# Optimization experiments

Hardware: AMD Instinct MI355X
Metric: run time of the kernel (lower is better)

The kernel has to match this reference:

```python
import jax, jax.numpy as jnp
import numpy as np

H = 1024
S = 8192
B = 1  # module's broadcast in the weighted-sum step only supports B == 1


def setup_inputs() -> dict:
    key = jax.random.key(0)
    k1, k2, k3 = jax.random.split(key, 3)
    scale = 1.0 / np.sqrt(H)
    enc_out = jax.random.normal(k1, (B, S, H), dtype=jnp.float32)
    w1 = jax.random.normal(k2, (H, H), dtype=jnp.float32) * scale  # nn.Linear weight [out,in]
    w2 = jax.random.normal(k3, (H, H), dtype=jnp.float32) * scale
    return {"enc_out": enc_out, "w1": w1, "w2": w2}


def reference(enc_out, w1, w2):
    # attn_weights = tanh(w1(enc_out)) @ w2(enc_out)^T  -> [B, S, S]
    q = jnp.tanh(jnp.einsum('bsh,oh->bso', enc_out, w1))
    k = jnp.einsum('bsh,oh->bso', enc_out, w2)
    scores = jnp.einsum('bih,bjh->bij', q, k)          # [B, S, S]
    attn = jax.nn.softmax(scores, axis=1)               # softmax over dim=1 (rows)
    # torch: sum over dim=1 of attn[B,S,S,1] * enc_out broadcast as [1,B,S,H].
    # For B==1 this equals enc_out[0,j,h] * sum_i attn[0,i,j]; avoid the
    # [B,S,S,H] intermediate the eager torch code materializes.
    col_sum = jnp.sum(attn, axis=1)                     # [B, S]
    context = col_sum[..., None] * enc_out              # [B, S, H]
    return context, attn
```

## Files before the change

### kernel.cpp

```cpp
#include <hip/hip_runtime.h>
#include <math.h>


typedef _Float16 half_t;
typedef _Float16 half8 __attribute__((ext_vector_type(8)));
typedef _Float16 half4 __attribute__((ext_vector_type(4)));
typedef float f32x4 __attribute__((ext_vector_type(4)));

#define S_DIM 8192
#define H_DIM 1024

__device__ __forceinline__ void gload16(const void* g, void* l) {
  __builtin_amdgcn_global_load_lds(
      (const __attribute__((address_space(1))) void*)g,
      (__attribute__((address_space(3))) void*)l, 16, 0, 0);
}

#define WAITVM(N) asm volatile("s_waitcnt vmcnt(" #N ")" ::: "memory")
#define BAR()                      \
  do {                             \
    asm volatile("" ::: "memory"); \
    __builtin_amdgcn_s_barrier();  \
    asm volatile("" ::: "memory"); \
  } while (0)

__global__ void __launch_bounds__(256) k_cvt(const float* __restrict__ src,
                                             half_t* __restrict__ dst) {
  long g = (long)blockIdx.x * 256 + threadIdx.x;
  f32x4 x = ((const f32x4*)src)[g];
  half4 h;
#pragma unroll
  for (int e = 0; e < 4; ++e) h[e] = (half_t)x[e];
  ((half4*)dst)[g] = h;
}

#define GEMM_MAINLOOP_8PH(APTR, BPTR)                                          \
  __shared__ __align__(16) half_t As[4][8192];                                 \
  __shared__ __align__(16) half_t Bs[4][8192];                                 \
  const int tid = threadIdx.x;                                                 \
  const int lane = tid & 63;                                                   \
  const int quad = lane >> 4;                                                  \
  const int l15 = lane & 15;                                                   \
  const int wave = tid >> 6;                                                   \
  const int wm = wave >> 2;                                          \
  const int wn = wave & 3;                                           \
  int aoff[2], boff[2], loff[2];                                               \
  _Pragma("unroll") for (int t = 0; t < 2; ++t) {                              \
    int f = t * 512 + tid;                                        \
    int u = f >> 8;                                                  \
    int m = f & 255;                                                           \
    aoff[t] = (bm * 256 + m) * H_DIM + u * 8;                                  \
    boff[t] = (bn * 256 + m) * H_DIM + u * 8;                                  \
    loff[t] = f * 8;                                                           \
  }                                                                            \
  f32x4 acc[8][4];                                                             \
  _Pragma("unroll") for (int r = 0; r < 8; ++r)                                \
      _Pragma("unroll") for (int c = 0; c < 4; ++c)                            \
          acc[r][c] = (f32x4){0.f, 0.f, 0.f, 0.f};                             \
                      \
  _Pragma("unroll") for (int pg = 0; pg < 3; ++pg) {                           \
    _Pragma("unroll") for (int t = 0; t < 2; ++t)                              \
        gload16(APTR + aoff[t] + pg * 32, &As[pg][loff[t]]);                   \
    _Pragma("unroll") for (int t = 0; t < 2; ++t)                              \
        gload16(BPTR + boff[t] + pg * 32, &Bs[pg][loff[t]]);                   \
  }                                                                            \
  WAITVM(4);               \
  BAR();                                                                       \
  const int arow = (quad * 256 + wm * 128 + l15) * 8;                          \
  const int brow = (quad * 256 + wn * 64 + l15) * 8;                           \
  _Pragma("unroll 1") for (int g = 0; g < 32; ++g) {                           \
    const half_t* Asl = As[g & 3];                                             \
    const half_t* Bsl = Bs[g & 3];                                             \
    half8 af[4], bf[4];                                                        \
                             \
    _Pragma("unroll") for (int r = 0; r < 4; ++r)                              \
        af[r] = *(const half8*)&Asl[arow + r * 128];                           \
    _Pragma("unroll") for (int c = 0; c < 4; ++c)                              \
        bf[c] = *(const half8*)&Bsl[brow + c * 128];                           \
    if (g + 3 < 32) {                 \
      const int ns = (g + 3) & 3;                                              \
      _Pragma("unroll") for (int t = 0; t < 2; ++t)                            \
          gload16(APTR + aoff[t] + (g + 3) * 32, &As[ns][loff[t]]);            \
    }                                                                          \
    BAR();                                                                     \
    __builtin_amdgcn_s_setprio(1);                                             \
    _Pragma("unroll") for (int r = 0; r < 4; ++r)                              \
        _Pragma("unroll") for (int c = 0; c < 4; ++c)                          \
            acc[r][c] = __builtin_amdgcn_mfma_f32_16x16x32_f16(                \
                af[r], bf[c], acc[r][c], 0, 0, 0);                             \
    __builtin_amdgcn_s_setprio(0);                                             \
    BAR();                                                                     \
                   \
    _Pragma("unroll") for (int r = 0; r < 4; ++r)                              \
        af[r] = *(const half8*)&Asl[arow + (r + 4) * 128];                     \
    if (g + 3 < 32) {                                   \
      const int ns = (g + 3) & 3;                                              \
      _Pragma("unroll") for (int t = 0; t < 2; ++t)                            \
          gload16(BPTR + boff[t] + (g + 3) * 32, &Bs[ns][loff[t]]);            \
    }                                                                          \
    BAR();                                                                     \
    __builtin_amdgcn_s_setprio(1);                                             \
    _Pragma("unroll") for (int r = 0; r < 4; ++r)                              \
        _Pragma("unroll") for (int c = 0; c < 4; ++c)                          \
            acc[r + 4][c] = __builtin_amdgcn_mfma_f32_16x16x32_f16(            \
                af[r], bf[c], acc[r + 4][c], 0, 0, 0);                         \
    __builtin_amdgcn_s_setprio(0);                                             \
    if (g & 1) {           \
      if (g < 27) { WAITVM(4); } else { WAITVM(0); }                           \
    }                                                                          \
    BAR();                                                                     \
  }

__global__ void __launch_bounds__(512, 2) k_gemm_qk(const half_t* __restrict__ A,
                                                    const half_t* __restrict__ B,
                                                    half_t* __restrict__ Qh,
                                                    half_t* __restrict__ Kh) {
  const int bm = blockIdx.y;
  const int bn = blockIdx.x;
  GEMM_MAINLOOP_8PH(A, B)
  const int colb = bn * 256 + wn * 64;
  const int rowb = bm * 256 + wm * 128;
  const bool isQ = (bn < 4);
#pragma unroll
  for (int r = 0; r < 8; ++r) {
#pragma unroll
    for (int c = 0; c < 4; ++c) {
      int col = colb + c * 16 + l15;
      int row = rowb + r * 16 + quad * 4;
      if (isQ) {
#pragma unroll
        for (int v = 0; v < 4; ++v)
          Qh[(long)(row + v) * 1024 + col] = (half_t)tanhf(acc[r][c][v]);
      } else {
#pragma unroll
        for (int v = 0; v < 4; ++v)
          Kh[(long)(row + v) * 1024 + (col - 1024)] = (half_t)acc[r][c][v];
      }
    }
  }
}

__global__ void __launch_bounds__(512, 2) k_stats(const half_t* __restrict__ A,
                                                  const half_t* __restrict__ B,
                                                  float* __restrict__ Pm,
                                                  float* __restrict__ Ps) {
  const int lin = blockIdx.x;
  const int patch = lin >> 6;
  const int local = lin & 63;
  const int bm = (patch >> 2) * 8 + (local >> 3);
  const int bn = (patch & 3) * 8 + (local & 7);
  GEMM_MAINLOOP_8PH(A, B)
  const int colb = bn * 256 + wn * 64;
  float cmax[4], csum[4];
#pragma unroll
  for (int c = 0; c < 4; ++c) {
    float m = acc[0][c][0];
#pragma unroll
    for (int r = 0; r < 8; ++r)
#pragma unroll
      for (int v = 0; v < 4; ++v) m = fmaxf(m, acc[r][c][v]);
    m = fmaxf(m, __shfl_xor(m, 16, 64));
    m = fmaxf(m, __shfl_xor(m, 32, 64));
    cmax[c] = m;
    float s = 0.f;
#pragma unroll
    for (int r = 0; r < 8; ++r)
#pragma unroll
      for (int v = 0; v < 4; ++v) s += __expf(acc[r][c][v] - m);
    s += __shfl_xor(s, 16, 64);
    s += __shfl_xor(s, 32, 64);
    csum[c] = s;
  }
  float* sred = (float*)As;
  if (quad == 0) {
#pragma unroll
    for (int c = 0; c < 4; ++c) {
      int idx = (((wm * 4 + wn) * 4 + c) * 16 + l15) * 2;
      sred[idx] = cmax[c];
      sred[idx + 1] = csum[c];
    }
  }
  __syncthreads();
  if (wm == 0 && quad == 0) {
#pragma unroll
    for (int c = 0; c < 4; ++c) {
      int i0 = (((0 * 4 + wn) * 4 + c) * 16 + l15) * 2;
      int i1 = (((1 * 4 + wn) * 4 + c) * 16 + l15) * 2;
      float m0 = sred[i0], s0 = sred[i0 + 1];
      float m1 = sred[i1], s1 = sred[i1 + 1];
      float M = fmaxf(m0, m1);
      float Ssum = s0 * __expf(m0 - M) + s1 * __expf(m1 - M);
      int col = colb + c * 16 + l15;
      Pm[(long)bm * S_DIM + col] = M;
      Ps[(long)bm * S_DIM + col] = Ssum;
    }
  }
}

__global__ void __launch_bounds__(256) k_combine(const float* __restrict__ Pm,
                                                 const float* __restrict__ Ps,
                                                 float* __restrict__ Mcol,
                                                 float* __restrict__ Rcol) {
  int j = blockIdx.x * 256 + threadIdx.x;
  float m = Pm[j];
  for (int r = 1; r < 32; ++r) m = fmaxf(m, Pm[(long)r * S_DIM + j]);
  float s = 0.f;
  for (int r = 0; r < 32; ++r)
    s += Ps[(long)r * S_DIM + j] * __expf(Pm[(long)r * S_DIM + j] - m);
  Mcol[j] = m;
  Rcol[j] = 1.0f / s;
}

__global__ void __launch_bounds__(512, 2) k_attn(const half_t* __restrict__ A,
                                                 const half_t* __restrict__ B,
                                                 const float* __restrict__ Mcol,
                                                 const float* __restrict__ Rcol,
                                                 float* __restrict__ out) {
  const int lin = blockIdx.x;
  const int patch = lin >> 6;
  const int local = lin & 63;
  const int bm = (patch >> 2) * 8 + (local >> 3);
  const int bn = (patch & 3) * 8 + (local & 7);
  GEMM_MAINLOOP_8PH(A, B)
  const int colb = bn * 256 + wn * 64;
  const int rowb = bm * 256 + wm * 128;
#pragma unroll
  for (int c = 0; c < 4; ++c) {
    int col = colb + c * 16 + l15;
    float M = Mcol[col];
    float R = Rcol[col];
#pragma unroll
    for (int r = 0; r < 8; ++r) {
      int row = rowb + r * 16 + quad * 4;
#pragma unroll
      for (int v = 0; v < 4; ++v) {
        out[(long)(row + v) * S_DIM + col] = __expf(acc[r][c][v] - M) * R;
      }
    }
  }
}

__global__ void __launch_bounds__(256) k_ctx(const f32x4* __restrict__ enc,
                                             f32x4* __restrict__ ctx) {
  long g = (long)blockIdx.x * 256 + threadIdx.x;
  ctx[g] = enc[g];
}

extern "C" void kernel_launch(void* const* d_in, const int* in_sizes, int n_in,
                              void* d_out, int out_size, void* d_ws, size_t ws_size,
                              hipStream_t stream) {
  const float* enc = (const float*)d_in[0];
  const float* w1 = (const float*)d_in[1];
  const float* w2 = (const float*)d_in[2];

  float* out = (float*)d_out;
  float* ctx = out;
  float* attn = out + 8388608;

  half_t* Qh = (half_t*)ctx;
  half_t* Kh = Qh + 8388608;
  half_t* enc_h = (half_t*)attn;
  half_t* w_h = (half_t*)((char*)attn + 16777216);
  float* Pm = attn + 8388608;
  float* Ps = Pm + 32 * S_DIM;
  float* Mcol = (float*)d_ws;
  float* Rcol = Mcol + S_DIM;

  k_cvt<<<8192, 256, 0, stream>>>(enc, enc_h);
  k_cvt<<<1024, 256, 0, stream>>>(w1, w_h);
  k_cvt<<<1024, 256, 0, stream>>>(w2, w_h + 1048576);

  k_gemm_qk<<<dim3(8, 32), 512, 0, stream>>>(enc_h, w_h, Qh, Kh);

  k_stats<<<1024, 512, 0, stream>>>(Qh, Kh, Pm, Ps);
  k_combine<<<32, 256, 0, stream>>>(Pm, Ps, Mcol, Rcol);

  k_attn<<<1024, 512, 0, stream>>>(Qh, Kh, Mcol, Rcol, attn);

  k_ctx<<<8192, 256, 0, stream>>>((const f32x4*)enc, (f32x4*)ctx);
}
```

Before: 725.0 us.

## Shrink GEMM tiles to 256x128 with 256-thread blocks and triple-buffered LDS

Replaces the 256x256, 512-thread GEMM mainloop with a 256x128 tile computed by 4 waves. The LDS ring drops from four stages to three, and the buffers rotate through pointer swaps. Explicit lgkmcnt waits with sched barriers are added before the MFMA phases. Grid sizes double for the QK, stats and attention kernels, which should help occupancy and load balance at the cost of re-reading A tiles more often and giving each block less arithmetic per load.

```diff
diff --git a/kernel.cpp b/kernel.cpp
--- a/kernel.cpp
+++ b/kernel.cpp
@@ -17,11 +17,11 @@
 }
 
 #define WAITVM(N) asm volatile("s_waitcnt vmcnt(" #N ")" ::: "memory")
-#define BAR()                      \
-  do {                             \
-    asm volatile("" ::: "memory"); \
-    __builtin_amdgcn_s_barrier();  \
-    asm volatile("" ::: "memory"); \
+#define BAR() asm volatile("s_barrier" ::: "memory")
+#define LGKM0()                                          \
+  do {                                                   \
+    asm volatile("s_waitcnt lgkmcnt(0)" ::: "memory");   \
+    __builtin_amdgcn_sched_barrier(0);                   \
   } while (0)
 
 __global__ void __launch_bounds__(256) k_cvt(const float* __restrict__ src,
@@ -34,55 +34,52 @@
   ((half4*)dst)[g] = h;
 }
 
-#define GEMM_MAINLOOP_8PH(APTR, BPTR)                                          \
-  __shared__ __align__(16) half_t As[4][8192];                                 \
-  __shared__ __align__(16) half_t Bs[4][8192];                                 \
+#define GEMM_MAINLOOP_T(APTR, BPTR)                                            \
+  __shared__ __align__(16) half_t As[3][8192];                                 \
+  __shared__ __align__(16) half_t Bs[3][4096];                                 \
   const int tid = threadIdx.x;                                                 \
   const int lane = tid & 63;                                                   \
   const int quad = lane >> 4;                                                  \
   const int l15 = lane & 15;                                                   \
   const int wave = tid >> 6;                                                   \
-  const int wm = wave >> 2;                                          \
-  const int wn = wave & 3;                                           \
-  int aoff[2], boff[2], loff[2];                                               \
-  _Pragma("unroll") for (int t = 0; t < 2; ++t) {                              \
-    int f = t * 512 + tid;                                        \
-    int u = f >> 8;                                                  \
-    int m = f & 255;                                                           \
-    aoff[t] = (bm * 256 + m) * H_DIM + u * 8;                                  \
-    boff[t] = (bn * 256 + m) * H_DIM + u * 8;                                  \
-    loff[t] = f * 8;                                                           \
-  }                                                                            \
+  const int wm = wave >> 1;                                          \
+  const int wn = wave & 1;                                           \
+  const int arow = (bm * 256 + tid) * H_DIM;                                   \
+  const int brow = (bn * 128 + (tid & 127)) * H_DIM;                           \
+  const int bu = (tid >> 7) * 8;                                               \
+  const int ldst = tid * 8;                                                    \
   f32x4 acc[8][4];                                                             \
   _Pragma("unroll") for (int r = 0; r < 8; ++r)                                \
       _Pragma("unroll") for (int c = 0; c < 4; ++c)                            \
           acc[r][c] = (f32x4){0.f, 0.f, 0.f, 0.f};                             \
-                      \
-  _Pragma("unroll") for (int pg = 0; pg < 3; ++pg) {                           \
-    _Pragma("unroll") for (int t = 0; t < 2; ++t)                              \
-        gload16(APTR + aoff[t] + pg * 32, &As[pg][loff[t]]);                   \
-    _Pragma("unroll") for (int t = 0; t < 2; ++t)                              \
-        gload16(BPTR + boff[t] + pg * 32, &Bs[pg][loff[t]]);                   \
-  }                                                                            \
-  WAITVM(4);               \
+  half_t *Ac = &As[0][0], *An = &As[1][0], *An2 = &As[2][0];                   \
+  half_t *Bc = &Bs[0][0], *Bn = &Bs[1][0], *Bn2 = &Bs[2][0];                   \
+                    \
+  _Pragma("unroll") for (int t = 0; t < 4; ++t)                                \
+      gload16(APTR + arow + t * 8, Ac + t * 2048 + ldst);                      \
+  _Pragma("unroll") for (int t = 0; t < 2; ++t)                                \
+      gload16(BPTR + brow + t * 16 + bu, Bc + t * 2048 + ldst);                \
+  _Pragma("unroll") for (int t = 0; t < 4; ++t)                                \
+      gload16(APTR + arow + 32 + t * 8, An + t * 2048 + ldst);                 \
+  _Pragma("unroll") for (int t = 0; t < 2; ++t)                                \
+      gload16(BPTR + brow + 32 + t * 16 + bu, Bn + t * 2048 + ldst);           \
+  WAITVM(6);                            \
   BAR();                                                                       \
-  const int arow = (quad * 256 + wm * 128 + l15) * 8;                          \
-  const int brow = (quad * 256 + wn * 64 + l15) * 8;                           \
+  const int abase = (quad * 256 + wm * 128 + l15) * 8;                         \
+  const int bbase = (quad * 128 + wn * 64 + l15) * 8;                          \
   _Pragma("unroll 1") for (int g = 0; g < 32; ++g) {                           \
-    const half_t* Asl = As[g & 3];                                             \
-    const half_t* Bsl = Bs[g & 3];                                             \
     half8 af[4], bf[4];                                                        \
-                             \
-    _Pragma("unroll") for (int r = 0; r < 4; ++r)                              \
-        af[r] = *(const half8*)&Asl[arow + r * 128];                           \
+                                       \
+    _Pragma("unroll") for (int r = 0; r < 4; ++r)                              \
+        af[r] = *(const half8*)&Ac[abase + r * 128];                           \
     _Pragma("unroll") for (int c = 0; c < 4; ++c)                              \
-        bf[c] = *(const half8*)&Bsl[brow + c * 128];                           \
-    if (g + 3 < 32) {                 \
-      const int ns = (g + 3) & 3;                                              \
-      _Pragma("unroll") for (int t = 0; t < 2; ++t)                            \
-          gload16(APTR + aoff[t] + (g + 3) * 32, &As[ns][loff[t]]);            \
+        bf[c] = *(const half8*)&Bc[bbase + c * 128];                           \
+    if (g + 2 < 32) {                                   \
+      _Pragma("unroll") for (int t = 0; t < 4; ++t)                            \
+          gload16(APTR + arow + (g + 2) * 32 + t * 8, An2 + t * 2048 + ldst);  \
     }                                                                          \
     BAR();                                                                     \
+    LGKM0();                                                                   \
     __builtin_amdgcn_s_setprio(1);                                             \
     _Pragma("unroll") for (int r = 0; r < 4; ++r)                              \
         _Pragma("unroll") for (int c = 0; c < 4; ++c)                          \
@@ -90,37 +87,40 @@
                 af[r], bf[c], acc[r][c], 0, 0, 0);                             \
     __builtin_amdgcn_s_setprio(0);                                             \
     BAR();                                                                     \
-                   \
-    _Pragma("unroll") for (int r = 0; r < 4; ++r)                              \
-        af[r] = *(const half8*)&Asl[arow + (r + 4) * 128];                     \
-    if (g + 3 < 32) {                                   \
-      const int ns = (g + 3) & 3;                                              \
+                             \
+    _Pragma("unroll") for (int r = 0; r < 4; ++r)                              \
+        af[r] = *(const half8*)&Ac[abase + (r + 4) * 128];                     \
+    if (g + 2 < 32) {                                   \
       _Pragma("unroll") for (int t = 0; t < 2; ++t)                            \
-          gload16(BPTR + boff[t] + (g + 3) * 32, &Bs[ns][loff[t]]);            \
+          gload16(BPTR + brow + (g + 2) * 32 + t * 16 + bu,                    \
+                  Bn2 + t * 2048 + ldst);                                      \
     }                                                                          \
     BAR();                                                                     \
+    LGKM0();                                                                   \
     __builtin_amdgcn_s_setprio(1);                                             \
     _Pragma("unroll") for (int r = 0; r < 4; ++r)                              \
         _Pragma("unroll") for (int c = 0; c < 4; ++c)                          \
             acc[r + 4][c] = __builtin_amdgcn_mfma_f32_16x16x32_f16(            \
                 af[r], bf[c], acc[r + 4][c], 0, 0, 0);                         \
     __builtin_amdgcn_s_setprio(0);                                             \
-    if (g & 1) {           \
-      if (g < 27) { WAITVM(4); } else { WAITVM(0); }                           \
-    }                                                                          \
-    BAR();                                                                     \
-  }
-
-__global__ void __launch_bounds__(512, 2) k_gemm_qk(const half_t* __restrict__ A,
+        \
+    if (g < 30) { WAITVM(6); }                                                 \
+    else if (g == 30) { WAITVM(0); }                                           \
+    BAR();                                                                     \
+    half_t* tA = Ac; Ac = An; An = An2; An2 = tA;                              \
+    half_t* tB = Bc; Bc = Bn; Bn = Bn2; Bn2 = tB;                              \
+  }
+
+__global__ void __launch_bounds__(256, 2) k_gemm_qk(const half_t* __restrict__ A,
                                                     const half_t* __restrict__ B,
                                                     half_t* __restrict__ Qh,
                                                     half_t* __restrict__ Kh) {
   const int bm = blockIdx.y;
   const int bn = blockIdx.x;
-  GEMM_MAINLOOP_8PH(A, B)
-  const int colb = bn * 256 + wn * 64;
+  GEMM_MAINLOOP_T(A, B)
+  const int colb = bn * 128 + wn * 64;
   const int rowb = bm * 256 + wm * 128;
-  const bool isQ = (bn < 4);
+  const bool isQ = (bn < 8);
 #pragma unroll
   for (int r = 0; r < 8; ++r) {
 #pragma unroll
@@ -140,17 +140,17 @@
   }
 }
 
-__global__ void __launch_bounds__(512, 2) k_stats(const half_t* __restrict__ A,
+__global__ void __launch_bounds__(256, 2) k_stats(const half_t* __restrict__ A,
                                                   const half_t* __restrict__ B,
                                                   float* __restrict__ Pm,
                                                   float* __restrict__ Ps) {
   const int lin = blockIdx.x;
   const int patch = lin >> 6;
   const int local = lin & 63;
-  const int bm = (patch >> 2) * 8 + (local >> 3);
-  const int bn = (patch & 3) * 8 + (local & 7);
-  GEMM_MAINLOOP_8PH(A, B)
-  const int colb = bn * 256 + wn * 64;
+  const int bm = (patch >> 3) * 8 + (local >> 3);
+  const int bn = (patch & 7) * 8 + (local & 7);
+  GEMM_MAINLOOP_T(A, B)
+  const int colb = bn * 128 + wn * 64;
   float cmax[4], csum[4];
 #pragma unroll
   for (int c = 0; c < 4; ++c) {
@@ -171,11 +171,12 @@
     s += __shfl_xor(s, 32, 64);
     csum[c] = s;
   }
+  __syncthreads();
   float* sred = (float*)As;
   if (quad == 0) {
 #pragma unroll
     for (int c = 0; c < 4; ++c) {
-      int idx = (((wm * 4 + wn) * 4 + c) * 16 + l15) * 2;
+      int idx = (((wm * 2 + wn) * 4 + c) * 16 + l15) * 2;
       sred[idx] = cmax[c];
       sred[idx + 1] = csum[c];
     }
@@ -184,8 +185,8 @@
   if (wm == 0 && quad == 0) {
 #pragma unroll
     for (int c = 0; c < 4; ++c) {
-      int i0 = (((0 * 4 + wn) * 4 + c) * 16 + l15) * 2;
-      int i1 = (((1 * 4 + wn) * 4 + c) * 16 + l15) * 2;
+      int i0 = (((0 * 2 + wn) * 4 + c) * 16 + l15) * 2;
+      int i1 = (((1 * 2 + wn) * 4 + c) * 16 + l15) * 2;
       float m0 = sred[i0], s0 = sred[i0 + 1];
       float m1 = sred[i1], s1 = sred[i1 + 1];
       float M = fmaxf(m0, m1);
@@ -211,7 +212,7 @@
   Rcol[j] = 1.0f / s;
 }
 
-__global__ void __launch_bounds__(512, 2) k_attn(const half_t* __restrict__ A,
+__global__ void __launch_bounds__(256, 2) k_attn(const half_t* __restrict__ A,
                                                  const half_t* __restrict__ B,
                                                  const float* __restrict__ Mcol,
                                                  const float* __restrict__ Rcol,
@@ -219,10 +220,10 @@
   const int lin = blockIdx.x;
   const int patch = lin >> 6;
   const int local = lin & 63;
-  const int bm = (patch >> 2) * 8 + (local >> 3);
-  const int bn = (patch & 3) * 8 + (local & 7);
-  GEMM_MAINLOOP_8PH(A, B)
-  const int colb = bn * 256 + wn * 64;
+  const int bm = (patch >> 3) * 8 + (local >> 3);
+  const int bn = (patch & 7) * 8 + (local & 7);
+  GEMM_MAINLOOP_T(A, B)
+  const int colb = bn * 128 + wn * 64;
   const int rowb = bm * 256 + wm * 128;
 #pragma unroll
   for (int c = 0; c < 4; ++c) {
@@ -270,12 +271,12 @@
   k_cvt<<<1024, 256, 0, stream>>>(w1, w_h);
   k_cvt<<<1024, 256, 0, stream>>>(w2, w_h + 1048576);
 
-  k_gemm_qk<<<dim3(8, 32), 512, 0, stream>>>(enc_h, w_h, Qh, Kh);
-
-  k_stats<<<1024, 512, 0, stream>>>(Qh, Kh, Pm, Ps);
+  k_gemm_qk<<<dim3(16, 32), 256, 0, stream>>>(enc_h, w_h, Qh, Kh);
+
+  k_stats<<<2048, 256, 0, stream>>>(Qh, Kh, Pm, Ps);
   k_combine<<<32, 256, 0, stream>>>(Pm, Ps, Mcol, Rcol);
 
-  k_attn<<<1024, 512, 0, stream>>>(Qh, Kh, Mcol, Rcol, attn);
+  k_attn<<<2048, 256, 0, stream>>>(Qh, Kh, Mcol, Rcol, attn);
 
   k_ctx<<<8192, 256, 0, stream>>>((const f32x4*)enc, (f32x4*)ctx);
 }
```

Result: slower. 786.6 us (+8.5%).
